# Optimization experiments

Measured on AMD Instinct MI355X. Metric: run time of the kernel, lower is better.

The kernel has to match this reference:

```python
import jax, jax.numpy as jnp
import numpy as np


def setup_inputs() -> dict:
    key = jax.random.key(0)
    kq, kk, kv = jax.random.split(key, 3)
    B, S, D = 4, 4096, 64
    q = jax.random.normal(kq, (B, S, D), dtype=jnp.float32)
    k = jax.random.normal(kk, (B, S, D), dtype=jnp.float32)
    v = jax.random.normal(kv, (B, S, D), dtype=jnp.float32)
    return {"q": q, "k": k, "v": v}


def reference(q, k, v):
    # q,k,v: [B,S,D]. Faithful to the torch module:
    #   attn = softmax(q @ k^T / sqrt(D))  -- softmax over full row (NOT pre-masked)
    #   attn = attn.masked_fill(tril==0, 0.0)  -- post-softmax causal zeroing
    #   out  = attn @ v
    S = q.shape[1]
    d = jnp.sqrt(jnp.asarray(q.shape[-1], dtype=q.dtype))
    scores = jnp.einsum("bqd,bkd->bqk", q, k) / d  # [B,S,S]
    attn = jax.nn.softmax(scores, axis=-1)
    # causal tril mask sliced from the registered buffer mask[:S,:S]
    causal = jnp.tril(jnp.ones((S, S), dtype=bool))  # [S,S]
    attn = jnp.where(causal[None, :, :], attn, jnp.asarray(0.0, dtype=attn.dtype))
    out = jnp.einsum("bqk,bkd->bqd", attn, v)  # [B,S,D]
    return out
```

## Files before the change

### kernel.cpp

```cpp
#include <hip/hip_runtime.h>
#include <math.h>


typedef _Float16 f16;
typedef __attribute__((ext_vector_type(8))) _Float16 f16x8;
typedef __attribute__((ext_vector_type(16))) float f32x16;

constexpr int S = 4096, D = 64, TK = 32;
constexpr int B_ = 4;
constexpr int NKT = S / TK;
constexpr int WPB = 8;
constexpr int TPW = 16;
constexpr int LDV = 40;
constexpr float QSC = 0.125f * 1.44269504088896340736f;

__global__ __launch_bounds__(256) void prep(
    const float* __restrict__ K, const float* __restrict__ V,
    f16* __restrict__ Kfrag, f16* __restrict__ Vfrag) {
  const int bx = blockIdx.x, tid = threadIdx.x;
  if (bx < B_ * NKT) {
    const float* src = K + (size_t)bx * TK * D;
    const int key = tid >> 3, j = tid & 7;
    float4 f0 = *reinterpret_cast<const float4*>(src + key * D + j * 8);
    float4 f1 = *reinterpret_cast<const float4*>(src + key * D + j * 8 + 4);
    f16x8 h;
    h[0] = (f16)f0.x; h[1] = (f16)f0.y; h[2] = (f16)f0.z; h[3] = (f16)f0.w;
    h[4] = (f16)f1.x; h[5] = (f16)f1.y; h[6] = (f16)f1.z; h[7] = (f16)f1.w;
    const int kc = j >> 1, h2 = j & 1;
    const int lane = key + 32 * h2;
    *reinterpret_cast<f16x8*>(Kfrag + ((size_t)bx * 4 + kc) * 512 + lane * 8) = h;
  } else {
    __shared__ float t32[TK][D + 4];
    const int vb = bx - B_ * NKT;
    const float* src = V + (size_t)vb * TK * D;
    #pragma unroll
    for (int r = 0; r < 2; ++r) {
      int f4 = tid + r * 256;
      int row = f4 >> 4, c4 = (f4 & 15) * 4;
      *reinterpret_cast<float4*>(&t32[row][c4]) =
          *reinterpret_cast<const float4*>(src + row * D + c4);
    }
    __syncthreads();
    const int dn = tid >> 7, kc2 = (tid >> 6) & 1, lane = tid & 63;
    const int l31 = lane & 31, h2 = lane >> 5;
    const int dim = dn * 32 + l31;
    const int k0 = kc2 * 16 + 8 * h2;
    f16x8 h;
    #pragma unroll
    for (int jj = 0; jj < 8; ++jj) h[jj] = (f16)t32[k0 + jj][dim];
    *reinterpret_cast<f16x8*>(
        Vfrag + ((size_t)vb * 4 + dn * 2 + kc2) * 512 + lane * 8) = h;
  }
}

__global__ __launch_bounds__(512, 2)
void attn(const float* __restrict__ Q, const f16* __restrict__ Kfrag,
          const f16* __restrict__ Vfrag, float* __restrict__ O) {
  __shared__ union {
    f16 ps[WPB][32][LDV];
    struct { float nb[4][32][68]; float db[WPB][32]; } r;
  } sm;

  const int i = blockIdx.x;
  const int b = (i & 7) >> 1;
  const int t = ((i >> 3) << 1) | (i & 1);
  const int qb = (t & 1) ? (127 - (t >> 1)) : (t >> 1);
  const int q0 = qb * TK;

  const int tid = threadIdx.x;
  const int w = tid >> 6, lane = tid & 63;
  const int l31 = lane & 31, h2 = lane >> 5;

  const size_t bSD = (size_t)b * S * D;

  f16x8 qh[4], qlo[4];
  {
    const float* qr = Q + bSD + (size_t)(q0 + l31) * D;
    #pragma unroll
    for (int kc = 0; kc < 4; ++kc) {
      float4 f0 = *reinterpret_cast<const float4*>(qr + kc * 16 + 8 * h2);
      float4 f1 = *reinterpret_cast<const float4*>(qr + kc * 16 + 8 * h2 + 4);
      float f[8] = {f0.x, f0.y, f0.z, f0.w, f1.x, f1.y, f1.z, f1.w};
      #pragma unroll
      for (int j = 0; j < 8; ++j) {
        float v = f[j] * QSC;
        f16 hi = (f16)v;
        qh[kc][j] = hi;
        qlo[kc][j] = (f16)(v - (float)hi);
      }
    }
  }

  const f16* kf = Kfrag + (size_t)b * NKT * 2048 + lane * 8;
  const f16* vf = Vfrag + (size_t)b * NKT * 2048 + lane * 8;

  f32x16 on0, on1;
  float ls[16];
  #pragma unroll
  for (int r = 0; r < 16; ++r) { on0[r] = 0.f; on1[r] = 0.f; ls[r] = 0.f; }

  f16x8 bk0, bk1, bk2, bk3, v00, v01, v10, v11;
  {
    const f16* kp = kf + (size_t)w * 2048;
    bk0 = *reinterpret_cast<const f16x8*>(kp);
    bk1 = *reinterpret_cast<const f16x8*>(kp + 512);
    bk2 = *reinterpret_cast<const f16x8*>(kp + 1024);
    bk3 = *reinterpret_cast<const f16x8*>(kp + 1536);
    if (w * TK <= q0) {
      const f16* vp = vf + (size_t)w * 2048;
      v00 = *reinterpret_cast<const f16x8*>(vp);
      v01 = *reinterpret_cast<const f16x8*>(vp + 512);
      v10 = *reinterpret_cast<const f16x8*>(vp + 1024);
      v11 = *reinterpret_cast<const f16x8*>(vp + 1536);
    }
  }

  for (int j = 0; j < TPW; ++j) {
    const int kt = (j << 3) | w;
    const int kbase = kt * TK;
    const bool pv = (kbase <= q0);
    const bool diag = (kbase == q0);

    f16x8 kn0, kn1, kn2, kn3, vn0, vn1, vn2, vn3;
    if (j + 1 < TPW) {
      const f16* kpn = kf + ((size_t)kt + 8) * 2048;
      kn0 = *reinterpret_cast<const f16x8*>(kpn);
      kn1 = *reinterpret_cast<const f16x8*>(kpn + 512);
      kn2 = *reinterpret_cast<const f16x8*>(kpn + 1024);
      kn3 = *reinterpret_cast<const f16x8*>(kpn + 1536);
      if ((kbase + 8 * TK) <= q0) {
        const f16* vpn = vf + ((size_t)kt + 8) * 2048;
        vn0 = *reinterpret_cast<const f16x8*>(vpn);
        vn1 = *reinterpret_cast<const f16x8*>(vpn + 512);
        vn2 = *reinterpret_cast<const f16x8*>(vpn + 1024);
        vn3 = *reinterpret_cast<const f16x8*>(vpn + 1536);
      }
    }

    f32x16 acc;
    #pragma unroll
    for (int r = 0; r < 16; ++r) acc[r] = 0.f;
    acc = __builtin_amdgcn_mfma_f32_32x32x16_f16(qlo[0], bk0, acc, 0, 0, 0);
    acc = __builtin_amdgcn_mfma_f32_32x32x16_f16(qh[0],  bk0, acc, 0, 0, 0);
    acc = __builtin_amdgcn_mfma_f32_32x32x16_f16(qlo[1], bk1, acc, 0, 0, 0);
    acc = __builtin_amdgcn_mfma_f32_32x32x16_f16(qh[1],  bk1, acc, 0, 0, 0);
    acc = __builtin_amdgcn_mfma_f32_32x32x16_f16(qlo[2], bk2, acc, 0, 0, 0);
    acc = __builtin_amdgcn_mfma_f32_32x32x16_f16(qh[2],  bk2, acc, 0, 0, 0);
    acc = __builtin_amdgcn_mfma_f32_32x32x16_f16(qlo[3], bk3, acc, 0, 0, 0);
    acc = __builtin_amdgcn_mfma_f32_32x32x16_f16(qh[3],  bk3, acc, 0, 0, 0);

    if (pv) {
      #pragma unroll
      for (int r = 0; r < 16; ++r) {
        float pp = __builtin_amdgcn_exp2f(acc[r]);
        f16 ph = (f16)pp;
        ls[r] += (float)ph;
        const int row = (r & 3) + 8 * (r >> 2) + 4 * h2;
        sm.ps[w][row][l31] = (!diag || l31 <= row) ? ph : (f16)0.f;
      }
    } else {
      #pragma unroll
      for (int r = 0; r < 16; ++r)
        ls[r] += __builtin_amdgcn_exp2f(acc[r]);
    }

    if (pv) {
      asm volatile("s_waitcnt lgkmcnt(0)" ::: "memory");
      f16x8 ap0 = *reinterpret_cast<const f16x8*>(&sm.ps[w][l31][8 * h2]);
      f16x8 ap1 = *reinterpret_cast<const f16x8*>(&sm.ps[w][l31][16 + 8 * h2]);
      on0 = __builtin_amdgcn_mfma_f32_32x32x16_f16(ap0, v00, on0, 0, 0, 0);
      on0 = __builtin_amdgcn_mfma_f32_32x32x16_f16(ap1, v01, on0, 0, 0, 0);
      on1 = __builtin_amdgcn_mfma_f32_32x32x16_f16(ap0, v10, on1, 0, 0, 0);
      on1 = __builtin_amdgcn_mfma_f32_32x32x16_f16(ap1, v11, on1, 0, 0, 0);
    }

    bk0 = kn0; bk1 = kn1; bk2 = kn2; bk3 = kn3;
    v00 = vn0; v01 = vn1; v10 = vn2; v11 = vn3;
  }

  #pragma unroll
  for (int r = 0; r < 16; ++r) {
    float v = ls[r];
    #pragma unroll
    for (int x = 1; x <= 16; x <<= 1) v += __shfl_xor(v, x);
    ls[r] = v;
  }
  __syncthreads();
  if (l31 == 0) {
    #pragma unroll
    for (int r = 0; r < 16; ++r)
      sm.r.db[w][(r & 3) + 8 * (r >> 2) + 4 * h2] = ls[r];
  }
  if (w < 4) {
    #pragma unroll
    for (int r = 0; r < 16; ++r) {
      const int row = (r & 3) + 8 * (r >> 2) + 4 * h2;
      sm.r.nb[w][row][l31]      = on0[r];
      sm.r.nb[w][row][32 + l31] = on1[r];
    }
  }
  __syncthreads();
  if (w >= 4) {
    #pragma unroll
    for (int r = 0; r < 16; ++r) {
      const int row = (r & 3) + 8 * (r >> 2) + 4 * h2;
      sm.r.nb[w - 4][row][l31]      += on0[r];
      sm.r.nb[w - 4][row][32 + l31] += on1[r];
    }
  }
  __syncthreads();

  const int row = tid >> 4, c4 = (tid & 15) * 4;
  float dsum = 0.f;
  #pragma unroll
  for (int ww = 0; ww < WPB; ++ww) dsum += sm.r.db[ww][row];
  const float inv = 1.f / dsum;
  float4 a0 = *reinterpret_cast<const float4*>(&sm.r.nb[0][row][c4]);
  float4 a1 = *reinterpret_cast<const float4*>(&sm.r.nb[1][row][c4]);
  float4 a2 = *reinterpret_cast<const float4*>(&sm.r.nb[2][row][c4]);
  float4 a3 = *reinterpret_cast<const float4*>(&sm.r.nb[3][row][c4]);
  float4 o;
  o.x = (a0.x + a1.x + a2.x + a3.x) * inv;
  o.y = (a0.y + a1.y + a2.y + a3.y) * inv;
  o.z = (a0.z + a1.z + a2.z + a3.z) * inv;
  o.w = (a0.w + a1.w + a2.w + a3.w) * inv;
  *reinterpret_cast<float4*>(O + bSD + (size_t)(q0 + row) * D + c4) = o;
}

extern "C" void kernel_launch(void* const* d_in, const int* in_sizes, int n_in,
                              void* d_out, int out_size, void* d_ws, size_t ws_size,
                              hipStream_t stream) {
  const float* q = (const float*)d_in[0];
  const float* k = (const float*)d_in[1];
  const float* v = (const float*)d_in[2];
  float* o = (float*)d_out;

  f16* Kfrag = (f16*)d_ws;
  f16* Vfrag = Kfrag + (size_t)B_ * S * D;

  prep<<<dim3(2 * B_ * NKT), dim3(256), 0, stream>>>(k, v, Kfrag, Vfrag);
  attn<<<dim3(512), dim3(512), 0, stream>>>(q, Kfrag, Vfrag, o);
}
```

Baseline: 104.3 us.

## Halve waves per attention block and load V tiles in-iteration instead of prefetching

Each block now uses 4 waves of 256 threads instead of 8 waves of 512, so every wave walks twice as many key tiles and the final cross-wave reduction and output store shrink or loop. V fragments are no longer prefetched one iteration ahead; they are loaded in the same iteration they are used, which frees registers. Launch bounds change to 256 threads with 3 blocks per CU to raise occupancy. The trade-off is less parallelism inside each block, a longer serial loop per wave, and exposed V-load latency.

```diff
diff --git a/kernel.cpp b/kernel.cpp
--- a/kernel.cpp
+++ b/kernel.cpp
@@ -9,8 +9,8 @@
 constexpr int S = 4096, D = 64, TK = 32;
 constexpr int B_ = 4;
 constexpr int NKT = S / TK;
-constexpr int WPB = 8;
-constexpr int TPW = 16;
+constexpr int WPB = 4;
+constexpr int TPW = NKT / WPB;
 constexpr int LDV = 40;
 constexpr float QSC = 0.125f * 1.44269504088896340736f;
 
@@ -53,12 +53,12 @@
   }
 }
 
-__global__ __launch_bounds__(512, 2)
+__global__ __launch_bounds__(256, 3)
 void attn(const float* __restrict__ Q, const f16* __restrict__ Kfrag,
           const f16* __restrict__ Vfrag, float* __restrict__ O) {
   __shared__ union {
     f16 ps[WPB][32][LDV];
-    struct { float nb[4][32][68]; float db[WPB][32]; } r;
+    struct { float nb[2][32][68]; float db[WPB][32]; } r;
   } sm;
 
   const int i = blockIdx.x;
@@ -99,42 +99,37 @@
   #pragma unroll
   for (int r = 0; r < 16; ++r) { on0[r] = 0.f; on1[r] = 0.f; ls[r] = 0.f; }
 
-  f16x8 bk0, bk1, bk2, bk3, v00, v01, v10, v11;
+  f16x8 bk0, bk1, bk2, bk3;
   {
     const f16* kp = kf + (size_t)w * 2048;
     bk0 = *reinterpret_cast<const f16x8*>(kp);
     bk1 = *reinterpret_cast<const f16x8*>(kp + 512);
     bk2 = *reinterpret_cast<const f16x8*>(kp + 1024);
     bk3 = *reinterpret_cast<const f16x8*>(kp + 1536);
-    if (w * TK <= q0) {
-      const f16* vp = vf + (size_t)w * 2048;
+  }
+
+  for (int j = 0; j < TPW; ++j) {
+    const int kt = (j << 2) | w;
+    const int kbase = kt * TK;
+    const bool pv = (kbase <= q0);
+    const bool diag = (kbase == q0);
+
+    f16x8 v00, v01, v10, v11;
+    if (pv) {
+      const f16* vp = vf + (size_t)kt * 2048;
       v00 = *reinterpret_cast<const f16x8*>(vp);
       v01 = *reinterpret_cast<const f16x8*>(vp + 512);
       v10 = *reinterpret_cast<const f16x8*>(vp + 1024);
       v11 = *reinterpret_cast<const f16x8*>(vp + 1536);
     }
-  }
-
-  for (int j = 0; j < TPW; ++j) {
-    const int kt = (j << 3) | w;
-    const int kbase = kt * TK;
-    const bool pv = (kbase <= q0);
-    const bool diag = (kbase == q0);
-
-    f16x8 kn0, kn1, kn2, kn3, vn0, vn1, vn2, vn3;
+
+    f16x8 kn0, kn1, kn2, kn3;
     if (j + 1 < TPW) {
-      const f16* kpn = kf + ((size_t)kt + 8) * 2048;
+      const f16* kpn = kf + ((size_t)kt + 4) * 2048;
       kn0 = *reinterpret_cast<const f16x8*>(kpn);
       kn1 = *reinterpret_cast<const f16x8*>(kpn + 512);
       kn2 = *reinterpret_cast<const f16x8*>(kpn + 1024);
       kn3 = *reinterpret_cast<const f16x8*>(kpn + 1536);
-      if ((kbase + 8 * TK) <= q0) {
-        const f16* vpn = vf + ((size_t)kt + 8) * 2048;
-        vn0 = *reinterpret_cast<const f16x8*>(vpn);
-        vn1 = *reinterpret_cast<const f16x8*>(vpn + 512);
-        vn2 = *reinterpret_cast<const f16x8*>(vpn + 1024);
-        vn3 = *reinterpret_cast<const f16x8*>(vpn + 1536);
-      }
     }
 
     f32x16 acc;
@@ -175,7 +170,6 @@
     }
 
     bk0 = kn0; bk1 = kn1; bk2 = kn2; bk3 = kn3;
-    v00 = vn0; v01 = vn1; v10 = vn2; v11 = vn3;
   }
 
   #pragma unroll
@@ -191,7 +185,7 @@
     for (int r = 0; r < 16; ++r)
       sm.r.db[w][(r & 3) + 8 * (r >> 2) + 4 * h2] = ls[r];
   }
-  if (w < 4) {
+  if (w < 2) {
     #pragma unroll
     for (int r = 0; r < 16; ++r) {
       const int row = (r & 3) + 8 * (r >> 2) + 4 * h2;
@@ -200,31 +194,33 @@
     }
   }
   __syncthreads();
-  if (w >= 4) {
+  if (w >= 2) {
     #pragma unroll
     for (int r = 0; r < 16; ++r) {
       const int row = (r & 3) + 8 * (r >> 2) + 4 * h2;
-      sm.r.nb[w - 4][row][l31]      += on0[r];
-      sm.r.nb[w - 4][row][32 + l31] += on1[r];
+      sm.r.nb[w - 2][row][l31]      += on0[r];
+      sm.r.nb[w - 2][row][32 + l31] += on1[r];
     }
   }
   __syncthreads();
 
-  const int row = tid >> 4, c4 = (tid & 15) * 4;
-  float dsum = 0.f;
   #pragma unroll
-  for (int ww = 0; ww < WPB; ++ww) dsum += sm.r.db[ww][row];
-  const float inv = 1.f / dsum;
-  float4 a0 = *reinterpret_cast<const float4*>(&sm.r.nb[0][row][c4]);
-  float4 a1 = *reinterpret_cast<const float4*>(&sm.r.nb[1][row][c4]);
-  float4 a2 = *reinterpret_cast<const float4*>(&sm.r.nb[2][row][c4]);
-  float4 a3 = *reinterpret_cast<const float4*>(&sm.r.nb[3][row][c4]);
-  float4 o;
-  o.x = (a0.x + a1.x + a2.x + a3.x) * inv;
-  o.y = (a0.y + a1.y + a2.y + a3.y) * inv;
-  o.z = (a0.z + a1.z + a2.z + a3.z) * inv;
-  o.w = (a0.w + a1.w + a2.w + a3.w) * inv;
-  *reinterpret_cast<float4*>(O + bSD + (size_t)(q0 + row) * D + c4) = o;
+  for (int it = 0; it < 2; ++it) {
+    const int i4 = tid + it * 256;
+    const int row = i4 >> 4, c4 = (i4 & 15) * 4;
+    float dsum = 0.f;
+    #pragma unroll
+    for (int ww = 0; ww < WPB; ++ww) dsum += sm.r.db[ww][row];
+    const float inv = 1.f / dsum;
+    float4 a0 = *reinterpret_cast<const float4*>(&sm.r.nb[0][row][c4]);
+    float4 a1 = *reinterpret_cast<const float4*>(&sm.r.nb[1][row][c4]);
+    float4 o;
+    o.x = (a0.x + a1.x) * inv;
+    o.y = (a0.y + a1.y) * inv;
+    o.z = (a0.z + a1.z) * inv;
+    o.w = (a0.w + a1.w) * inv;
+    *reinterpret_cast<float4*>(O + bSD + (size_t)(q0 + row) * D + c4) = o;
+  }
 }
 
 extern "C" void kernel_launch(void* const* d_in, const int* in_sizes, int n_in,
@@ -239,5 +235,5 @@
   f16* Vfrag = Kfrag + (size_t)B_ * S * D;
 
   prep<<<dim3(2 * B_ * NKT), dim3(256), 0, stream>>>(k, v, Kfrag, Vfrag);
-  attn<<<dim3(512), dim3(512), 0, stream>>>(q, Kfrag, Vfrag, o);
+  attn<<<dim3(512), dim3(256), 0, stream>>>(q, Kfrag, Vfrag, o);
 }
```

Result: faster. 97.77 us (-6.3%).
